# Optimization experiments

Measured on AMD Instinct MI355X. Metric: run time of the kernel, lower is better.

Reference implementation:

```python
import jax, jax.numpy as jnp
import numpy as np

E = 1024
H = 16
D = E // H  # head_dim = 64
B, L, S = 2, 2048, 2048


def setup_inputs() -> dict:
    key = jax.random.key(0)
    ks = jax.random.split(key, 10)
    scale = 1.0 / np.sqrt(E)
    return {
        "x": jax.random.normal(ks[0], (B, L, E), jnp.float32),
        "context": jax.random.normal(ks[1], (B, S, E), jnp.float32),
        "Wq": jax.random.normal(ks[2], (E, E), jnp.float32) * scale,
        "bq": jnp.zeros((E,), jnp.float32),
        "Wk": jax.random.normal(ks[3], (E, E), jnp.float32) * scale,
        "bk": jnp.zeros((E,), jnp.float32),
        "Wv": jax.random.normal(ks[4], (E, E), jnp.float32) * scale,
        "bv": jnp.zeros((E,), jnp.float32),
        "Wp": jax.random.normal(ks[5], (E, E), jnp.float32) * scale,
        "bp": jnp.zeros((E,), jnp.float32),
    }


def reference(x, context, Wq, bq, Wk, bk, Wv, bv, Wp, bp):
    b, l, _ = x.shape
    s = context.shape[1]
    # linear projections then split heads: [B, H, L/S, D]
    q = (x @ Wq + bq).reshape(b, l, H, D).transpose(0, 2, 1, 3)
    k = (context @ Wk + bk).reshape(b, s, H, D).transpose(0, 2, 1, 3)
    v = (context @ Wv + bv).reshape(b, s, H, D).transpose(0, 2, 1, 3)
    # scores [B, H, L, S]
    attn = jnp.einsum("bhld,bhsd->bhls", q, k) / jnp.sqrt(jnp.float32(D))
    attn = jax.nn.softmax(attn, axis=-1)
    # dropout is identity in eval mode
    out = jnp.einsum("bhls,bhsd->bhld", attn, v)
    out = out.transpose(0, 2, 1, 3).reshape(b, l, E)
    return out @ Wp + bp
```

## Files before the change

kernel.cpp:

```cpp
#include <hip/hip_runtime.h>
#include <math.h>

#define B_ 2
#define L_ 2048
#define S_ 2048
#define E_ 1024
#define H_ 16
#define D_ 64
#define SC_ 0.180336880111120f

typedef unsigned short u16;
typedef unsigned int u32;
typedef __attribute__((ext_vector_type(8))) short short8;
typedef __attribute__((ext_vector_type(4))) float floatx4;

__device__ __forceinline__ u16 f2bf(float f) {
    union { float f; unsigned u; } a; a.f = f;
    unsigned r = a.u + 0x7FFFu + ((a.u >> 16) & 1u);
    return (u16)(r >> 16);
}

__device__ __forceinline__ u32 cvt_pk_bf16(float lo, float hi) {
    u32 d;
    asm("v_cvt_pk_bf16_f32 %0, %1, %2" : "=v"(d) : "v"(lo), "v"(hi));
    return d;
}

__device__ __forceinline__ void pl32swap(u32& a, u32& b) {
    asm("v_permlane32_swap_b32 %0, %1" : "+v"(a), "+v"(b));
}
__device__ __forceinline__ void pl16swap(u32& a, u32& b) {
    asm("v_permlane16_swap_b32 %0, %1" : "+v"(a), "+v"(b));
}

__device__ __forceinline__ void glds16(const u16* g, u16* l) {
    __builtin_amdgcn_global_load_lds(
        (const __attribute__((address_space(1))) void*)g,
        (__attribute__((address_space(3))) void*)l, 16, 0, 0);
}

__global__ void prep_kernel(const float* __restrict__ x, const float* __restrict__ ctx,
                            u16* __restrict__ Xb, u16* __restrict__ Cb,
                            const float* __restrict__ Wq, const float* __restrict__ Wk,
                            const float* __restrict__ Wv, const float* __restrict__ Wp,
                            u16* __restrict__ WqT, u16* __restrict__ WkT,
                            u16* __restrict__ WvT, u16* __restrict__ WpT) {
    __shared__ float tile[32][33];
    const int bid = blockIdx.x;
    const int tid = threadIdx.x;
    if (bid < 4096) {
        const int sub = bid;
        const float* src = sub < 2048 ? x : ctx;
        u16* dst = sub < 2048 ? Xb : Cb;
        int i = (sub & 2047) * 256 + tid;
        float4 u0 = ((const float4*)src)[2 * i];
        float4 u1 = ((const float4*)src)[2 * i + 1];
        uint4 o;
        o.x = cvt_pk_bf16(u0.x, u0.y);
        o.y = cvt_pk_bf16(u0.z, u0.w);
        o.z = cvt_pk_bf16(u1.x, u1.y);
        o.w = cvt_pk_bf16(u1.z, u1.w);
        ((uint4*)dst)[i] = o;
    } else {
        const int t = bid - 4096;
        const int z = t >> 10;
        const int rem = t & 1023;
        const float* W = z == 0 ? Wq : (z == 1 ? Wk : (z == 2 ? Wv : Wp));
        u16* Wt = z == 0 ? WqT : (z == 1 ? WkT : (z == 2 ? WvT : WpT));
        const int bx = (rem & 31) * 32, by = (rem >> 5) * 32;
        const int tx = tid & 31, ty = tid >> 5;
#pragma unroll
        for (int j = 0; j < 4; ++j)
            tile[ty + j * 8][tx] = W[(size_t)(by + ty + j * 8) * E_ + bx + tx];
        __syncthreads();
#pragma unroll
        for (int j = 0; j < 4; ++j)
            Wt[(size_t)(bx + ty + j * 8) * E_ + by + tx] = f2bf(tile[tx][ty + j * 8]);
    }
}

__device__ __forceinline__ void xcd_remap64(int bx, int by, int& m_idx, int& n_idx) {
    int lin = bx + 8 * by;
    int c8 = lin & 7;
    int g = lin >> 3;
    m_idx = c8 + 8 * (g & 7);
    n_idx = g >> 3;
}

__global__ __launch_bounds__(256, 2) void qkv_gemm_kernel(
    const u16* __restrict__ Xb, const u16* __restrict__ Cb,
    const u16* __restrict__ WqT, const u16* __restrict__ WkT, const u16* __restrict__ WvT,
    const float* __restrict__ bq, const float* __restrict__ bk, const float* __restrict__ bv,
    u16* __restrict__ Qb, u16* __restrict__ Kb, u16* __restrict__ Vtb) {
    __shared__ __align__(16) u16 sm[40960];

    const int z = blockIdx.z;
    const u16* A   = z == 0 ? Xb : Cb;
    const u16* Btk = z == 0 ? WqT : WkT;

    const int tid = threadIdx.x;
    const int lane = tid & 63;
    const int wv = tid >> 6;
    const int wm = wv >> 1, wn = wv & 1;
    const int qd = lane >> 4, lr = lane & 15;
    int m_idx, n_idx;
    xcd_remap64(blockIdx.x, blockIdx.y, m_idx, n_idx);
    const int m0 = m_idx * 64, n0 = n_idx * 128;
    const int lrow = lane >> 3;
    const int gu = (lane & 7) ^ lrow;

    floatx4 acck[2][4], accv[2][4];
#pragma unroll
    for (int i = 0; i < 2; ++i)
#pragma unroll
        for (int j = 0; j < 4; ++j) {
            floatx4 zz = {0.f, 0.f, 0.f, 0.f};
            acck[i][j] = zz;
            accv[i][j] = zz;
        }

#define STAGE_AB(buf, kb)                                                          \
    {                                                                              \
        _Pragma("unroll") for (int j = 0; j < 2; ++j) {                            \
            int c = wv * 2 + j;                                                    \
            glds16(A + (size_t)(m0 + c * 8 + lrow) * E_ + (kb) + gu * 8,           \
                   sm + (buf)*4096 + c * 512);                                     \
        }                                                                          \
        _Pragma("unroll") for (int j = 0; j < 4; ++j) {                            \
            int c = wv * 4 + j;                                                    \
            glds16(Btk + (size_t)(n0 + c * 8 + lrow) * E_ + (kb) + gu * 8,         \
                   sm + 8192 + (buf)*8192 + c * 512);                              \
        }                                                                          \
        if (z == 1) {                                                              \
            _Pragma("unroll") for (int j = 0; j < 4; ++j) {                        \
                int c = wv * 4 + j;                                                \
                glds16(WvT + (size_t)(n0 + c * 8 + lrow) * E_ + (kb) + gu * 8,     \
                       sm + 24576 + (buf)*8192 + c * 512);                         \
            }                                                                      \
        }                                                                          \
    }

    STAGE_AB(0, 0)
    __syncthreads();

    for (int t = 0; t < 16; ++t) {
        const int cur = t & 1;
        if (t + 1 < 16) STAGE_AB(cur ^ 1, (t + 1) * 64)

        short8 af[2][2];
#pragma unroll
        for (int mi = 0; mi < 2; ++mi)
#pragma unroll
            for (int kk = 0; kk < 2; ++kk) {
                int row = wm * 32 + mi * 16 + lr;
                int u = (kk * 4 + qd) ^ (lr & 7);
                af[mi][kk] = *(const short8*)(sm + cur * 4096 + row * 64 + u * 8);
            }
        {
            short8 bfk[4][2];
#pragma unroll
            for (int ni = 0; ni < 4; ++ni)
#pragma unroll
                for (int kk = 0; kk < 2; ++kk) {
                    int row = wn * 64 + ni * 16 + lr;
                    int u = (kk * 4 + qd) ^ (lr & 7);
                    bfk[ni][kk] = *(const short8*)(sm + 8192 + cur * 8192 + row * 64 + u * 8);
                }
            __builtin_amdgcn_s_setprio(1);
#pragma unroll
            for (int kk = 0; kk < 2; ++kk)
#pragma unroll
                for (int mi = 0; mi < 2; ++mi)
#pragma unroll
                    for (int ni = 0; ni < 4; ++ni)
                        acck[mi][ni] = __builtin_amdgcn_mfma_f32_16x16x32_bf16(
                            af[mi][kk], bfk[ni][kk], acck[mi][ni], 0, 0, 0);
            __builtin_amdgcn_s_setprio(0);
        }
        if (z == 1) {
            short8 bfv[4][2];
#pragma unroll
            for (int ni = 0; ni < 4; ++ni)
#pragma unroll
                for (int kk = 0; kk < 2; ++kk) {
                    int row = wn * 64 + ni * 16 + lr;
                    int u = (kk * 4 + qd) ^ (lr & 7);
                    bfv[ni][kk] = *(const short8*)(sm + 24576 + cur * 8192 + row * 64 + u * 8);
                }
            __builtin_amdgcn_s_setprio(1);
#pragma unroll
            for (int kk = 0; kk < 2; ++kk)
#pragma unroll
                for (int mi = 0; mi < 2; ++mi)
#pragma unroll
                    for (int ni = 0; ni < 4; ++ni)
                        accv[mi][ni] = __builtin_amdgcn_mfma_f32_16x16x32_bf16(
                            af[mi][kk], bfv[ni][kk], accv[mi][ni], 0, 0, 0);
            __builtin_amdgcn_s_setprio(0);
        }

        __syncthreads();
    }

    if (z == 0) {
#pragma unroll
        for (int mi = 0; mi < 2; ++mi)
#pragma unroll
            for (int ni = 0; ni < 4; ++ni) {
                int col = n0 + wn * 64 + ni * 16 + lr;
                float bv_ = bq[col];
#pragma unroll
                for (int r = 0; r < 4; ++r) {
                    int row = m0 + wm * 32 + mi * 16 + qd * 4 + r;
                    Qb[(size_t)row * E_ + col] = f2bf((acck[mi][ni][r] + bv_) * SC_);
                }
            }
    } else {
#pragma unroll
        for (int mi = 0; mi < 2; ++mi)
#pragma unroll
            for (int ni = 0; ni < 4; ++ni) {
                int col = n0 + wn * 64 + ni * 16 + lr;
                float bv_ = bk[col];
#pragma unroll
                for (int r = 0; r < 4; ++r) {
                    int row = m0 + wm * 32 + mi * 16 + qd * 4 + r;
                    Kb[(size_t)row * E_ + col] = f2bf(acck[mi][ni][r] + bv_);
                }
            }
        const int CTS = 72;
#pragma unroll
        for (int mi = 0; mi < 2; ++mi)
#pragma unroll
            for (int ni = 0; ni < 4; ++ni) {
                int col = wn * 64 + ni * 16 + lr;
                int row = wm * 32 + mi * 16 + qd * 4;
                float bv_ = bv[n0 + col];
                u16 h0 = f2bf(accv[mi][ni][0] + bv_);
                u16 h1 = f2bf(accv[mi][ni][1] + bv_);
                u16 h2 = f2bf(accv[mi][ni][2] + bv_);
                u16 h3 = f2bf(accv[mi][ni][3] + bv_);
                uint2 pk;
                pk.x = h0 | ((u32)h1 << 16);
                pk.y = h2 | ((u32)h3 << 16);
                *(uint2*)&sm[col * CTS + row] = pk;
            }
        __syncthreads();
        const int d = tid >> 1;
        const int sh = (tid & 1) * 32;
        const int bidx = m0 >> 11;
        const int sloc = m0 & (S_ - 1);
        u16* dstV = Vtb + ((size_t)(bidx * E_ + n0 + d)) * S_ + sloc + sh;
        const u16* srcC = sm + d * CTS + sh;
#pragma unroll
        for (int j = 0; j < 4; ++j)
            *(uint4*)(dstV + j * 8) = *(const uint4*)(srcC + j * 8);
    }
#undef STAGE_AB
}

__global__ __launch_bounds__(256, 4) void flash_attn_kernel(
    const u16* __restrict__ Q, const u16* __restrict__ Kg,
    const u16* __restrict__ Vtg, u16* __restrict__ Opart, float* __restrict__ lpart) {
    __shared__ __align__(16) u16 Ks[2][64 * 64];
    __shared__ __align__(16) u16 Vs[2][64 * 64];

    const int tid = threadIdx.x;
    const int lane = tid & 63;
    const int wv = tid >> 6;
    const int qd = lane >> 4, lr = lane & 15;

    const int lin = blockIdx.x + 16 * (blockIdx.y + 32 * blockIdx.z);
    const int c8 = lin & 7;
    const int slot = lin >> 3;
    const int qx = slot & 15;
    const int grp = c8 + 8 * (slot >> 4);
    const int bh = grp & 31;
    const int z = grp >> 5;
    const int b = bh >> 4, h = bh & 15;
    const int q0 = qx * 128;
    const int sbeg = z * (S_ / 2);

    u16* Op = Opart + (size_t)z * (B_ * L_ * E_);
    float* lp = lpart + (size_t)z * (B_ * H_ * L_);

    const u16* Kbase = Kg + (size_t)(b * S_) * E_ + h * D_;
    const u16* Vbase = Vtg + (size_t)(b * E_ + h * D_) * S_;

    const int lrow = lane >> 3;
    const int gu = (lane & 7) ^ lrow;

#pragma unroll
    for (int j = 0; j < 2; ++j) {
        int c = wv * 2 + j;
        glds16(Kbase + (size_t)(sbeg + c * 8 + lrow) * E_ + gu * 8, &Ks[0][c * 512]);
        glds16(Vbase + (size_t)(c * 8 + lrow) * S_ + sbeg + gu * 8, &Vs[0][c * 512]);
    }

    short8 qf[2][2];
#pragma unroll
    for (int mi = 0; mi < 2; ++mi)
#pragma unroll
        for (int kk = 0; kk < 2; ++kk)
            qf[mi][kk] = *(const short8*)(Q + (size_t)(b * L_ + q0 + wv * 32 + mi * 16 + lr) * E_ +
                                          h * D_ + kk * 32 + qd * 8);

    const short one_bf = (short)0x3F80;
    short8 ones8 = {one_bf, one_bf, one_bf, one_bf, one_bf, one_bf, one_bf, one_bf};

    floatx4 o_acc[2][4];
    floatx4 l4[2];
#pragma unroll
    for (int mi = 0; mi < 2; ++mi) {
#pragma unroll
        for (int nt = 0; nt < 4; ++nt) {
            floatx4 z4 = {0.f, 0.f, 0.f, 0.f};
            o_acc[mi][nt] = z4;
        }
        floatx4 z4 = {0.f, 0.f, 0.f, 0.f};
        l4[mi] = z4;
    }

    __syncthreads();

    const int NIT = (S_ / 2) / 64;

    for (int it = 0; it < NIT; ++it) {
        const int cur = it & 1;
        if (it + 1 < NIT) {
            int s1 = sbeg + (it + 1) * 64;
#pragma unroll
            for (int j = 0; j < 2; ++j) {
                int c = wv * 2 + j;
                glds16(Kbase + (size_t)(s1 + c * 8 + lrow) * E_ + gu * 8, &Ks[cur ^ 1][c * 512]);
                glds16(Vbase + (size_t)(c * 8 + lrow) * S_ + s1 + gu * 8, &Vs[cur ^ 1][c * 512]);
            }
        }

        floatx4 s_[2][4];
        __builtin_amdgcn_s_setprio(1);
#pragma unroll
        for (int nt = 0; nt < 4; ++nt) {
            int krow = nt * 16 + lr;
            short8 kb0 = *(const short8*)(&Ks[cur][krow * 64 + ((qd) ^ (lr & 7)) * 8]);
            short8 kb1 = *(const short8*)(&Ks[cur][krow * 64 + ((4 + qd) ^ (lr & 7)) * 8]);
#pragma unroll
            for (int mi = 0; mi < 2; ++mi) {
                floatx4 zz = {0.f, 0.f, 0.f, 0.f};
                zz = __builtin_amdgcn_mfma_f32_16x16x32_bf16(kb0, qf[mi][0], zz, 0, 0, 0);
                zz = __builtin_amdgcn_mfma_f32_16x16x32_bf16(kb1, qf[mi][1], zz, 0, 0, 0);
                s_[mi][nt] = zz;
            }
        }
        __builtin_amdgcn_s_setprio(0);

        short8 pf[2][2];
#pragma unroll
        for (int mi = 0; mi < 2; ++mi) {
            u32 dg[4][2];
#pragma unroll
            for (int nt = 0; nt < 4; ++nt) {
                float p0 = __builtin_amdgcn_exp2f(s_[mi][nt][0]);
                float p1 = __builtin_amdgcn_exp2f(s_[mi][nt][1]);
                float p2 = __builtin_amdgcn_exp2f(s_[mi][nt][2]);
                float p3 = __builtin_amdgcn_exp2f(s_[mi][nt][3]);
                dg[nt][0] = cvt_pk_bf16(p0, p1);
                dg[nt][1] = cvt_pk_bf16(p2, p3);
            }
#pragma unroll
            for (int kk = 0; kk < 2; ++kk) {
                u32 x0 = dg[2 * kk][0], y0 = dg[2 * kk + 1][0];
                pl32swap(x0, y0);
                pl16swap(x0, y0);
                u32 x1 = dg[2 * kk][1], y1 = dg[2 * kk + 1][1];
                pl32swap(x1, y1);
                pl16swap(x1, y1);
                union { u32 d[4]; short8 v; } u;
                u.d[0] = x0; u.d[1] = x1; u.d[2] = y0; u.d[3] = y1;
                pf[mi][kk] = u.v;
            }
        }

        __builtin_amdgcn_s_setprio(1);
#pragma unroll
        for (int mi = 0; mi < 2; ++mi) {
            l4[mi] = __builtin_amdgcn_mfma_f32_16x16x32_bf16(pf[mi][0], ones8, l4[mi], 0, 0, 0);
            l4[mi] = __builtin_amdgcn_mfma_f32_16x16x32_bf16(pf[mi][1], ones8, l4[mi], 0, 0, 0);
        }
#pragma unroll
        for (int nt = 0; nt < 4; ++nt) {
            int vrow = nt * 16 + lr;
            short8 vb0 = *(const short8*)(&Vs[cur][vrow * 64 + ((qd) ^ (lr & 7)) * 8]);
            short8 vb1 = *(const short8*)(&Vs[cur][vrow * 64 + ((4 + qd) ^ (lr & 7)) * 8]);
#pragma unroll
            for (int mi = 0; mi < 2; ++mi) {
                o_acc[mi][nt] = __builtin_amdgcn_mfma_f32_16x16x32_bf16(pf[mi][0], vb0, o_acc[mi][nt], 0, 0, 0);
                o_acc[mi][nt] = __builtin_amdgcn_mfma_f32_16x16x32_bf16(pf[mi][1], vb1, o_acc[mi][nt], 0, 0, 0);
            }
        }
        __builtin_amdgcn_s_setprio(0);

        __syncthreads();
    }

    float linv[2][4];
#pragma unroll
    for (int mi = 0; mi < 2; ++mi) {
        if (lr == 0) {
#pragma unroll
            for (int r = 0; r < 4; ++r)
                lp[(size_t)(b * H_ + h) * L_ + q0 + wv * 32 + mi * 16 + qd * 4 + r] = l4[mi][r];
        }
#pragma unroll
        for (int r = 0; r < 4; ++r) linv[mi][r] = 1.0f / l4[mi][r];
    }

#pragma unroll
    for (int mi = 0; mi < 2; ++mi)
#pragma unroll
        for (int nt = 0; nt < 4; ++nt)
#pragma unroll
            for (int r = 0; r < 4; ++r) {
                int row = q0 + wv * 32 + mi * 16 + qd * 4 + r;
                int col = h * D_ + nt * 16 + lr;
                Op[(size_t)(b * L_ + row) * E_ + col] = f2bf(o_acc[mi][nt][r] * linv[mi][r]);
            }
}

__global__ __launch_bounds__(256, 2) void out_gemm_kernel(
    const u16* __restrict__ O1, const u16* __restrict__ O2,
    const float* __restrict__ l1, const float* __restrict__ l2,
    const u16* __restrict__ WpT, const float* __restrict__ bp,
    float* __restrict__ out) {
    __shared__ __align__(16) u16 As[2][64 * 64];
    __shared__ __align__(16) u16 Bs[2][128 * 64];

    const int tid = threadIdx.x;
    const int lane = tid & 63;
    const int wv = tid >> 6;
    const int wm = wv >> 1, wn = wv & 1;
    const int qd = lane >> 4, lr = lane & 15;

    int m_idx, n_idx;
    xcd_remap64(blockIdx.x, blockIdx.y, m_idx, n_idx);
    const int m0 = m_idx * 64, n0 = n_idx * 128;
    const int lrow = lane >> 3;
    const int gu = (lane & 7) ^ lrow;

    floatx4 acc[2][4];
#pragma unroll
    for (int i = 0; i < 2; ++i)
#pragma unroll
        for (int j = 0; j < 4; ++j) {
            floatx4 zz = {0.f, 0.f, 0.f, 0.f};
            acc[i][j] = zz;
        }

    uint4 p1[2], p2[2];
    float la_[2], lb_[2];

#define LOAD_AO(tt)                                                                \
    {                                                                              \
        _Pragma("unroll") for (int j = 0; j < 2; ++j) {                            \
            int c = wv * 2 + j;                                                    \
            int row = m0 + c * 8 + lrow;                                           \
            int col = (tt)*64 + gu * 8;                                            \
            p1[j] = *(const uint4*)(O1 + (size_t)row * E_ + col);                  \
            p2[j] = *(const uint4*)(O2 + (size_t)row * E_ + col);                  \
            int li = (row >> 11) * (H_ * L_) + (tt)*L_ + (row & (L_ - 1));         \
            la_[j] = l1[li];                                                       \
            lb_[j] = l2[li];                                                       \
        }                                                                          \
    }

#define WRITE_AO(buf)                                                              \
    {                                                                              \
        _Pragma("unroll") for (int j = 0; j < 2; ++j) {                            \
            int c = wv * 2 + j;                                                    \
            float s = 1.0f / (la_[j] + lb_[j]);                                    \
            float w1 = la_[j] * s, w2 = lb_[j] * s;                                \
            const u32* pa = (const u32*)&p1[j];                                    \
            const u32* pb = (const u32*)&p2[j];                                    \
            uint4 o;                                                               \
            u32* po = (u32*)&o;                                                    \
            _Pragma("unroll") for (int d = 0; d < 4; ++d) {                        \
                union { u32 u; float f; } x0, x1, y0, y1;                          \
                x0.u = pa[d] << 16; x1.u = pa[d] & 0xFFFF0000u;                    \
                y0.u = pb[d] << 16; y1.u = pb[d] & 0xFFFF0000u;                    \
                po[d] = cvt_pk_bf16(x0.f * w1 + y0.f * w2, x1.f * w1 + y1.f * w2); \
            }                                                                      \
            *(uint4*)(&As[buf][c * 512 + lane * 8]) = o;                           \
        }                                                                          \
    }

#define STAGE_BO(buf, kb)                                                          \
    {                                                                              \
        _Pragma("unroll") for (int j = 0; j < 4; ++j) {                            \
            int c = wv * 4 + j;                                                    \
            glds16(WpT + (size_t)(n0 + c * 8 + lrow) * E_ + (kb) + gu * 8,         \
                   &Bs[buf][c * 512]);                                             \
        }                                                                          \
    }

    LOAD_AO(0)
    STAGE_BO(0, 0)
    WRITE_AO(0)
    __syncthreads();

    for (int t = 0; t < 16; ++t) {
        const int cur = t & 1;
        if (t + 1 < 16) {
            STAGE_BO(cur ^ 1, (t + 1) * 64)
            LOAD_AO(t + 1)
        }

        short8 af[2][2], bf[4][2];
#pragma unroll
        for (int mi = 0; mi < 2; ++mi)
#pragma unroll
            for (int kk = 0; kk < 2; ++kk) {
                int row = wm * 32 + mi * 16 + lr;
                int u = (kk * 4 + qd) ^ (lr & 7);
                af[mi][kk] = *(const short8*)(&As[cur][row * 64 + u * 8]);
            }
#pragma unroll
        for (int ni = 0; ni < 4; ++ni)
#pragma unroll
            for (int kk = 0; kk < 2; ++kk) {
                int row = wn * 64 + ni * 16 + lr;
                int u = (kk * 4 + qd) ^ (lr & 7);
                bf[ni][kk] = *(const short8*)(&Bs[cur][row * 64 + u * 8]);
            }
        __builtin_amdgcn_s_setprio(1);
#pragma unroll
        for (int kk = 0; kk < 2; ++kk)
#pragma unroll
            for (int mi = 0; mi < 2; ++mi)
#pragma unroll
                for (int ni = 0; ni < 4; ++ni)
                    acc[mi][ni] = __builtin_amdgcn_mfma_f32_16x16x32_bf16(
                        af[mi][kk], bf[ni][kk], acc[mi][ni], 0, 0, 0);
        __builtin_amdgcn_s_setprio(0);

        if (t + 1 < 16) WRITE_AO(cur ^ 1)
        __syncthreads();
    }

#pragma unroll
    for (int mi = 0; mi < 2; ++mi)
#pragma unroll
        for (int ni = 0; ni < 4; ++ni) {
            int col = n0 + wn * 64 + ni * 16 + lr;
            float bv_ = bp[col];
#pragma unroll
            for (int r = 0; r < 4; ++r) {
                int row = m0 + wm * 32 + mi * 16 + qd * 4 + r;
                out[(size_t)row * E_ + col] = acc[mi][ni][r] + bv_;
            }
        }
#undef LOAD_AO
#undef WRITE_AO
#undef STAGE_BO
}

extern "C" void kernel_launch(void* const* d_in, const int* in_sizes, int n_in,
                              void* d_out, int out_size, void* d_ws, size_t ws_size,
                              hipStream_t stream) {
    const float* x   = (const float*)d_in[0];
    const float* ctx = (const float*)d_in[1];
    const float* Wq  = (const float*)d_in[2];
    const float* bq  = (const float*)d_in[3];
    const float* Wk  = (const float*)d_in[4];
    const float* bk  = (const float*)d_in[5];
    const float* Wv  = (const float*)d_in[6];
    const float* bv  = (const float*)d_in[7];
    const float* Wp  = (const float*)d_in[8];
    const float* bp  = (const float*)d_in[9];
    float* out = (float*)d_out;

    u16* WqT = (u16*)d_ws;
    u16* WkT = WqT + 1048576;
    u16* WvT = WkT + 1048576;
    u16* WpT = WvT + 1048576;
    u16* Qb  = WpT + 1048576;
    u16* Kb  = Qb + 4194304;
    u16* Vtb = Kb + 4194304;
    u16* Xb  = Vtb + 4194304;
    u16* Cb  = Xb + 4194304;
    u16* Opart = Xb;
    float* lpart = (float*)(Cb + 4194304);
    (void)ws_size; (void)in_sizes; (void)n_in; (void)out_size;

    prep_kernel<<<dim3(8192), 256, 0, stream>>>(
        x, ctx, Xb, Cb, Wq, Wk, Wv, Wp, WqT, WkT, WvT, WpT);

    qkv_gemm_kernel<<<dim3(8, 64, 2), 256, 0, stream>>>(
        Xb, Cb, WqT, WkT, WvT, bq, bk, bv, Qb, Kb, Vtb);

    flash_attn_kernel<<<dim3(L_ / 128, B_ * H_, 2), 256, 0, stream>>>(
        Qb, Kb, Vtb, Opart, lpart);

    out_gemm_kernel<<<dim3(8, 64), 256, 0, stream>>>(
        Opart, Opart + 4194304, lpart, lpart + B_ * H_ * L_, WpT, bp, out);
}
```

Baseline: 198.8 us.

## Fuse fp32-to-bf16 activation conversion into QKV GEMM A-tile staging

```diff
diff --git a/kernel.cpp b/kernel.cpp
--- a/kernel.cpp
+++ b/kernel.cpp
@@ -39,44 +39,26 @@
         (__attribute__((address_space(3))) void*)l, 16, 0, 0);
 }
 
-__global__ void prep_kernel(const float* __restrict__ x, const float* __restrict__ ctx,
-                            u16* __restrict__ Xb, u16* __restrict__ Cb,
-                            const float* __restrict__ Wq, const float* __restrict__ Wk,
+__global__ void prep_kernel(const float* __restrict__ Wq, const float* __restrict__ Wk,
                             const float* __restrict__ Wv, const float* __restrict__ Wp,
                             u16* __restrict__ WqT, u16* __restrict__ WkT,
                             u16* __restrict__ WvT, u16* __restrict__ WpT) {
     __shared__ float tile[32][33];
-    const int bid = blockIdx.x;
+    const int t = blockIdx.x;
     const int tid = threadIdx.x;
-    if (bid < 4096) {
-        const int sub = bid;
-        const float* src = sub < 2048 ? x : ctx;
-        u16* dst = sub < 2048 ? Xb : Cb;
-        int i = (sub & 2047) * 256 + tid;
-        float4 u0 = ((const float4*)src)[2 * i];
-        float4 u1 = ((const float4*)src)[2 * i + 1];
-        uint4 o;
-        o.x = cvt_pk_bf16(u0.x, u0.y);
-        o.y = cvt_pk_bf16(u0.z, u0.w);
-        o.z = cvt_pk_bf16(u1.x, u1.y);
-        o.w = cvt_pk_bf16(u1.z, u1.w);
-        ((uint4*)dst)[i] = o;
-    } else {
-        const int t = bid - 4096;
-        const int z = t >> 10;
-        const int rem = t & 1023;
-        const float* W = z == 0 ? Wq : (z == 1 ? Wk : (z == 2 ? Wv : Wp));
-        u16* Wt = z == 0 ? WqT : (z == 1 ? WkT : (z == 2 ? WvT : WpT));
-        const int bx = (rem & 31) * 32, by = (rem >> 5) * 32;
-        const int tx = tid & 31, ty = tid >> 5;
-#pragma unroll
-        for (int j = 0; j < 4; ++j)
-            tile[ty + j * 8][tx] = W[(size_t)(by + ty + j * 8) * E_ + bx + tx];
-        __syncthreads();
-#pragma unroll
-        for (int j = 0; j < 4; ++j)
-            Wt[(size_t)(bx + ty + j * 8) * E_ + by + tx] = f2bf(tile[tx][ty + j * 8]);
-    }
+    const int z = t >> 10;
+    const int rem = t & 1023;
+    const float* W = z == 0 ? Wq : (z == 1 ? Wk : (z == 2 ? Wv : Wp));
+    u16* Wt = z == 0 ? WqT : (z == 1 ? WkT : (z == 2 ? WvT : WpT));
+    const int bx = (rem & 31) * 32, by = (rem >> 5) * 32;
+    const int tx = tid & 31, ty = tid >> 5;
+#pragma unroll
+    for (int j = 0; j < 4; ++j)
+        tile[ty + j * 8][tx] = W[(size_t)(by + ty + j * 8) * E_ + bx + tx];
+    __syncthreads();
+#pragma unroll
+    for (int j = 0; j < 4; ++j)
+        Wt[(size_t)(bx + ty + j * 8) * E_ + by + tx] = f2bf(tile[tx][ty + j * 8]);
 }
 
 __device__ __forceinline__ void xcd_remap64(int bx, int by, int& m_idx, int& n_idx) {
@@ -88,15 +70,15 @@
 }
 
 __global__ __launch_bounds__(256, 2) void qkv_gemm_kernel(
-    const u16* __restrict__ Xb, const u16* __restrict__ Cb,
+    const float* __restrict__ x, const float* __restrict__ ctx,
     const u16* __restrict__ WqT, const u16* __restrict__ WkT, const u16* __restrict__ WvT,
     const float* __restrict__ bq, const float* __restrict__ bk, const float* __restrict__ bv,
     u16* __restrict__ Qb, u16* __restrict__ Kb, u16* __restrict__ Vtb) {
     __shared__ __align__(16) u16 sm[40960];
 
     const int z = blockIdx.z;
-    const u16* A   = z == 0 ? Xb : Cb;
-    const u16* Btk = z == 0 ? WqT : WkT;
+    const float* Af = z == 0 ? x : ctx;
+    const u16* Btk  = z == 0 ? WqT : WkT;
 
     const int tid = threadIdx.x;
     const int lane = tid & 63;
@@ -119,13 +101,33 @@
             accv[i][j] = zz;
         }
 
-#define STAGE_AB(buf, kb)                                                          \
+    float4 alo[2], ahi[2];
+
+#define STAGE_A_LOAD(kb)                                                           \
     {                                                                              \
         _Pragma("unroll") for (int j = 0; j < 2; ++j) {                            \
             int c = wv * 2 + j;                                                    \
-            glds16(A + (size_t)(m0 + c * 8 + lrow) * E_ + (kb) + gu * 8,           \
-                   sm + (buf)*4096 + c * 512);                                     \
+            const float* src = Af + (size_t)(m0 + c * 8 + lrow) * E_ + (kb) + gu * 8; \
+            alo[j] = *(const float4*)src;                                          \
+            ahi[j] = *(const float4*)(src + 4);                                    \
         }                                                                          \
+    }
+
+#define STAGE_A_WRITE(buf)                                                         \
+    {                                                                              \
+        _Pragma("unroll") for (int j = 0; j < 2; ++j) {                            \
+            int c = wv * 2 + j;                                                    \
+            uint4 o;                                                               \
+            o.x = cvt_pk_bf16(alo[j].x, alo[j].y);                                 \
+            o.y = cvt_pk_bf16(alo[j].z, alo[j].w);                                 \
+            o.z = cvt_pk_bf16(ahi[j].x, ahi[j].y);                                 \
+            o.w = cvt_pk_bf16(ahi[j].z, ahi[j].w);                                 \
+            *(uint4*)&sm[(buf)*4096 + c * 512 + lane * 8] = o;                     \
+        }                                                                          \
+    }
+
+#define STAGE_B(buf, kb)                                                           \
+    {                                                                              \
         _Pragma("unroll") for (int j = 0; j < 4; ++j) {                            \
             int c = wv * 4 + j;                                                    \
             glds16(Btk + (size_t)(n0 + c * 8 + lrow) * E_ + (kb) + gu * 8,         \
@@ -140,12 +142,17 @@
         }                                                                          \
     }
 
-    STAGE_AB(0, 0)
+    STAGE_A_LOAD(0)
+    STAGE_B(0, 0)
+    STAGE_A_WRITE(0)
     __syncthreads();
 
     for (int t = 0; t < 16; ++t) {
         const int cur = t & 1;
-        if (t + 1 < 16) STAGE_AB(cur ^ 1, (t + 1) * 64)
+        if (t + 1 < 16) {
+            STAGE_B(cur ^ 1, (t + 1) * 64)
+            STAGE_A_LOAD((t + 1) * 64)
+        }
 
         short8 af[2][2];
 #pragma unroll
@@ -199,6 +206,7 @@
             __builtin_amdgcn_s_setprio(0);
         }
 
+        if (t + 1 < 16) STAGE_A_WRITE(cur ^ 1)
         __syncthreads();
     }
 
@@ -229,6 +237,7 @@
                 }
             }
         const int CTS = 72;
+        __syncthreads();
 #pragma unroll
         for (int mi = 0; mi < 2; ++mi)
 #pragma unroll
@@ -256,7 +265,9 @@
         for (int j = 0; j < 4; ++j)
             *(uint4*)(dstV + j * 8) = *(const uint4*)(srcC + j * 8);
     }
-#undef STAGE_AB
+#undef STAGE_A_LOAD
+#undef STAGE_A_WRITE
+#undef STAGE_B
 }
 
 __global__ __launch_bounds__(256, 4) void flash_attn_kernel(
@@ -585,17 +596,15 @@
     u16* Qb  = WpT + 1048576;
     u16* Kb  = Qb + 4194304;
     u16* Vtb = Kb + 4194304;
-    u16* Xb  = Vtb + 4194304;
-    u16* Cb  = Xb + 4194304;
-    u16* Opart = Xb;
-    float* lpart = (float*)(Cb + 4194304);
+    u16* Opart = Vtb + 4194304;
+    float* lpart = (float*)(Opart + 2 * 4194304);
     (void)ws_size; (void)in_sizes; (void)n_in; (void)out_size;
 
-    prep_kernel<<<dim3(8192), 256, 0, stream>>>(
-        x, ctx, Xb, Cb, Wq, Wk, Wv, Wp, WqT, WkT, WvT, WpT);
+    prep_kernel<<<dim3(4096), 256, 0, stream>>>(
+        Wq, Wk, Wv, Wp, WqT, WkT, WvT, WpT);
 
     qkv_gemm_kernel<<<dim3(8, 64, 2), 256, 0, stream>>>(
-        Xb, Cb, WqT, WkT, WvT, bq, bk, bv, Qb, Kb, Vtb);
+        x, ctx, WqT, WkT, WvT, bq, bk, bv, Qb, Kb, Vtb);
 
     flash_attn_kernel<<<dim3(L_ / 128, B_ * H_, 2), 256, 0, stream>>>(
         Qb, Kb, Vtb, Opart, lpart);
```

Result: slower. 209.3 us (+5.2%).
